# Kernel tuning notes

Hardware: AMD Instinct MI355X
Metric: run time of the kernel (lower is better)

Reference implementation:

```python
import jax, jax.numpy as jnp
import numpy as np

N_NODES = 100000
N_EDGES = 1600000
D_IN, D_HID, D_OUT = 64, 64, 32


def _glorot(key, shape):
    fan_in = shape[0]
    return jax.random.normal(key, shape, dtype=jnp.float32) / np.sqrt(fan_in)


def setup_inputs() -> dict:
    key = jax.random.key(0)
    ks = jax.random.split(key, 12)
    x = jax.random.normal(ks[0], (N_NODES, D_IN), dtype=jnp.float32)
    edge_index = jax.random.randint(ks[1], (2, N_EDGES), 0, N_NODES, dtype=jnp.int32)
    dims = [(D_IN, D_HID), (D_HID, D_HID), (D_HID, D_OUT)]
    params = {}
    for i, (din, dout) in enumerate(dims):
        params[f"Wl{i}"] = _glorot(ks[2 + 3 * i], (din, dout))
        params[f"Wr{i}"] = _glorot(ks[3 + 3 * i], (din, dout))
        params[f"b{i}"] = jnp.zeros((dout,), dtype=jnp.float32)
    return {"x": x, "edge_index": edge_index, **params}


def _sage_conv(h, src, dst, deg_inv, Wl, Wr, b):
    # mean-aggregate neighbor features: gather from src, scatter-sum to dst
    msg_sum = jax.ops.segment_sum(h[src], dst, num_segments=N_NODES)  # [N, F]
    mean = msg_sum * deg_inv[:, None]
    # lin_l(mean) + bias + lin_r(h)  (PyG SAGEConv: bias lives in lin_l)
    return mean @ Wl + b + h @ Wr


def reference(x, edge_index, Wl0, Wr0, b0, Wl1, Wr1, b1, Wl2, Wr2, b2):
    src, dst = edge_index[0], edge_index[1]
    deg = jax.ops.segment_sum(jnp.ones((N_EDGES,), x.dtype), dst, num_segments=N_NODES)
    deg_inv = 1.0 / jnp.maximum(deg, 1.0)  # mean with clamp for isolated nodes
    h = jax.nn.elu(_sage_conv(x, src, dst, deg_inv, Wl0, Wr0, b0))
    h = jax.nn.elu(_sage_conv(h, src, dst, deg_inv, Wl1, Wr1, b1))
    return _sage_conv(h, src, dst, deg_inv, Wl2, Wr2, b2)
```

## Files before the change

kernel.cpp:

```cpp
#include <hip/hip_runtime.h>
#include <cstdint>
#include <cstddef>


constexpr int SBW = 256;
constexpr int LOGSBW = 8;
constexpr int CAPS = 4608;
constexpr int CAPSP = 5632;
constexpr int CHK = 2048;

typedef __attribute__((ext_vector_type(8))) short s16x8;
typedef __attribute__((ext_vector_type(4))) float f32x4;
typedef __attribute__((ext_vector_type(2))) float f32x2;

__device__ inline unsigned short f2bf(float f) {
  unsigned u = __builtin_bit_cast(unsigned, f);
  u += 0x7FFFu + ((u >> 16) & 1u);
  return (unsigned short)(u >> 16);
}
__device__ inline float bf2f(unsigned short b) {
  unsigned u = ((unsigned)b) << 16;
  return __builtin_bit_cast(float, u);
}
__device__ inline unsigned char f2fp8(float f) {
  int p = __builtin_amdgcn_cvt_pk_fp8_f32(f, f, 0, false);
  return (unsigned char)(p & 0xFF);
}


__global__ __launch_bounds__(256) void init_ws(int* __restrict__ bcur, int NSB,
                                               const float* __restrict__ Wl0,
                                               const float* __restrict__ Wr0,
                                               const float* __restrict__ Wl1,
                                               const float* __restrict__ Wr1,
                                               const float* __restrict__ Wl2,
                                               const float* __restrict__ Wr2,
                                               unsigned short* __restrict__ Wsw) {
  const int tid = threadIdx.x;
  if (blockIdx.x == 0) {
    for (int i = tid; i < NSB; i += 256) bcur[i] = 0;
    return;
  }
  int g = (blockIdx.x - 1) * 256 + tid;
  if (g >= 10240) return;
  int s = g * 2;
  int layer, off;
  if (s < 8192)       { layer = 0; off = 0; }
  else if (s < 16384) { layer = 1; off = 8192; }
  else                { layer = 2; off = 16384; }
  int t = s - off;
  int D = (layer == 2) ? 32 : 64;
  int NTT = D / 16;
  int tt = t >> 10;
  int rem = t & 1023;
  int plane = rem >> 9;
  int rem2 = rem & 511;
  int lane = rem2 >> 3;
  int j = rem2 & 7;
  int q = lane >> 4, m = lane & 15;
  int k = plane * 32 + q * 8 + j;
  const float* W;
  int c;
  if (tt < NTT) {
    c = tt;
    W = (layer == 0) ? Wl0 : (layer == 1) ? Wl1 : Wl2;
  } else {
    c = tt - NTT;
    W = (layer == 0) ? Wr0 : (layer == 1) ? Wr1 : Wr2;
  }
  int col = c * 16 + m;
  unsigned lo = f2bf(W[k * D + col]);
  unsigned hi = f2bf(W[(k + 1) * D + col]);
  *(unsigned*)&Wsw[s] = lo | (hi << 16);
}


__global__ __launch_bounds__(256) void bin_coarse(const int* __restrict__ src,
                                                  const int* __restrict__ dst,
                                                  int* __restrict__ bcur,
                                                  unsigned int* __restrict__ coarse,
                                                  int NSB, int E) {
  __shared__ int h[512];
  __shared__ unsigned ed[CHK];
  __shared__ short sb[CHK];
  const int tid = threadIdx.x;
  for (int i = tid; i < NSB; i += 256) h[i] = 0;
  __syncthreads();
  const int e0 = blockIdx.x * CHK;
  const int e1 = min(E, e0 + CHK);
  for (int e = e0 + tid; e < e1; e += 256) {
    int d = dst[e];
    int s = src[e];
    int b = d >> LOGSBW;
    ed[e - e0] = (unsigned)s | ((unsigned)(d & (SBW - 1)) << 17);
    sb[e - e0] = (short)b;
    atomicAdd(&h[b], 1);
  }
  __syncthreads();
  for (int i = tid; i < NSB; i += 256) {
    int c = h[i];
    h[i] = c ? (i * CAPS + atomicAdd(&bcur[i], c)) : 0;
  }
  __syncthreads();
  const int n = e1 - e0;
  for (int k = tid; k < n; k += 256) {
    int b = sb[k];
    int pos = atomicAdd(&h[b], 1);
    if (pos < (b + 1) * CAPS)
      coarse[pos] = ed[k];
  }
}


__global__ __launch_bounds__(256) void csr_gemm0(const unsigned int* __restrict__ coarse,
                                                 const int* __restrict__ bcur,
                                                 int* __restrict__ rowstart,
                                                 int* __restrict__ degarr,
                                                 float* __restrict__ deg_inv,
                                                 int* __restrict__ colidx,
                                                 const float* __restrict__ x,
                                                 const unsigned short* __restrict__ Wf,
                                                 const float* __restrict__ bias,
                                                 unsigned char* __restrict__ t_out,
                                                 unsigned short* __restrict__ r_out,
                                                 int N, int NSB) {
  __shared__ int cnt[SBW];
  __shared__ int sc[SBW];
  __shared__ int cur[SBW];
  const int tid = threadIdx.x;
  if ((int)blockIdx.x < NSB) {
    const int b = blockIdx.x;
    cnt[tid] = 0;
    __syncthreads();
    const int ec = min(bcur[b], CAPS);
    const int baseC = b * CAPS;
    const int baseP = b * CAPSP;
    for (int e = tid; e < ec; e += 256)
      atomicAdd(&cnt[coarse[baseC + e] >> 17], 1);
    __syncthreads();
    int v = cnt[tid];
    int pc = (v + 3) & ~3;
    sc[tid] = pc;
    __syncthreads();
    for (int off = 1; off < SBW; off <<= 1) {
      int y = sc[tid];
      if (tid >= off) y += sc[tid - off];
      __syncthreads();
      sc[tid] = y;
      __syncthreads();
    }
    int pex = sc[tid] - pc;
    cur[tid] = pex;
    int gn = b * SBW + tid;
    if (gn < N) {
      rowstart[gn] = baseP + pex;
      degarr[gn] = pc;
      deg_inv[gn] = 1.0f / (float)(v > 1 ? v : 1);
    }
    __syncthreads();
    for (int e = tid; e < ec; e += 256) {
      unsigned p = coarse[baseC + e];
      int dl = (int)(p >> 17);
      int s = (int)(p & 0x1FFFFu);
      int l = atomicAdd(&cur[dl], 1);
      if (l < CAPSP)
        colidx[baseP + l] = s;
    }
    int pe = pex + pc;
    if (pe > CAPSP) pe = CAPSP;
    for (int l = pex + v; l < pe; ++l) colidx[baseP + l] = N;
    return;
  }
  constexpr int DOUT = 64;
  constexpr int NTT = 4;
  const int gbid = blockIdx.x - NSB;
  if (gbid == 0 && tid < 16)
    ((unsigned*)t_out)[(size_t)N * 16 + tid] = 0u;
  const int wv = tid >> 6, lane = tid & 63;
  const int q = lane >> 4, m = lane & 15;
  const int row = gbid * 64 + wv * 16 + m;
  const int rowc = row < N ? row : N - 1;
  const float* xp = &x[(size_t)rowc * 64];
  float4 f0 = *(const float4*)&xp[q * 8];
  float4 f1 = *(const float4*)&xp[q * 8 + 4];
  float4 f2 = *(const float4*)&xp[32 + q * 8];
  float4 f3 = *(const float4*)&xp[32 + q * 8 + 4];
  s16x8 a0, a1;
  a0[0] = (short)f2bf(f0.x); a0[1] = (short)f2bf(f0.y);
  a0[2] = (short)f2bf(f0.z); a0[3] = (short)f2bf(f0.w);
  a0[4] = (short)f2bf(f1.x); a0[5] = (short)f2bf(f1.y);
  a0[6] = (short)f2bf(f1.z); a0[7] = (short)f2bf(f1.w);
  a1[0] = (short)f2bf(f2.x); a1[1] = (short)f2bf(f2.y);
  a1[2] = (short)f2bf(f2.z); a1[3] = (short)f2bf(f2.w);
  a1[4] = (short)f2bf(f3.x); a1[5] = (short)f2bf(f3.y);
  a1[6] = (short)f2bf(f3.z); a1[7] = (short)f2bf(f3.w);

  f32x4 acc[2 * NTT];
#pragma unroll
  for (int c = 0; c < 2 * NTT; ++c) acc[c] = (f32x4){0.f, 0.f, 0.f, 0.f};
#pragma unroll
  for (int c = 0; c < 2 * NTT; ++c) {
    s16x8 b0 = *(const s16x8*)&Wf[(c * 2 + 0) * 512 + lane * 8];
    s16x8 b1 = *(const s16x8*)&Wf[(c * 2 + 1) * 512 + lane * 8];
    acc[c] = __builtin_amdgcn_mfma_f32_16x16x32_bf16(a0, b0, acc[c], 0, 0, 0);
    acc[c] = __builtin_amdgcn_mfma_f32_16x16x32_bf16(a1, b1, acc[c], 0, 0, 0);
  }

  const int orow = gbid * 64 + wv * 16 + q * 4;
#pragma unroll
  for (int c = 0; c < NTT; ++c) {
#pragma unroll
    for (int i = 0; i < 4; ++i) {
      int r_ = orow + i;
      if (r_ < N) t_out[(size_t)r_ * DOUT + c * 16 + m] = f2fp8(acc[c][i]);
    }
  }
#pragma unroll
  for (int c = 0; c < NTT; ++c) {
    float bv = bias[c * 16 + m];
#pragma unroll
    for (int i = 0; i < 4; ++i) {
      int r_ = orow + i;
      if (r_ < N) r_out[(size_t)r_ * DOUT + c * 16 + m] = f2bf(acc[NTT + c][i] + bv);
    }
  }
}


template <int DOUT, bool TFP8, bool RB16>
__global__ __launch_bounds__(256) void gemm_mfma(const unsigned short* __restrict__ Hm,
                                                 const unsigned short* __restrict__ Wf,
                                                 const float* __restrict__ bias,
                                                 void* __restrict__ t_out,
                                                 void* __restrict__ r_out, int N) {
  constexpr int NTT = DOUT / 16;
  constexpr int ROWB = TFP8 ? DOUT : DOUT * 2;
  const int tid = threadIdx.x;
  if (blockIdx.x == 0 && tid < ROWB / 4)
    ((unsigned*)((char*)t_out + (size_t)N * ROWB))[tid] = 0u;
  const int wv = tid >> 6, lane = tid & 63;
  const int q = lane >> 4, m = lane & 15;
  const int row = blockIdx.x * 64 + wv * 16 + m;
  const int rowc = row < N ? row : N - 1;
  const s16x8 a0 = *(const s16x8*)&Hm[(size_t)rowc * 64 + q * 8];
  const s16x8 a1 = *(const s16x8*)&Hm[(size_t)rowc * 64 + 32 + q * 8];

  f32x4 acc[2 * NTT];
#pragma unroll
  for (int c = 0; c < 2 * NTT; ++c) acc[c] = (f32x4){0.f, 0.f, 0.f, 0.f};
#pragma unroll
  for (int c = 0; c < 2 * NTT; ++c) {
    s16x8 b0 = *(const s16x8*)&Wf[(c * 2 + 0) * 512 + lane * 8];
    s16x8 b1 = *(const s16x8*)&Wf[(c * 2 + 1) * 512 + lane * 8];
    acc[c] = __builtin_amdgcn_mfma_f32_16x16x32_bf16(a0, b0, acc[c], 0, 0, 0);
    acc[c] = __builtin_amdgcn_mfma_f32_16x16x32_bf16(a1, b1, acc[c], 0, 0, 0);
  }

  const int orow = blockIdx.x * 64 + wv * 16 + q * 4;
#pragma unroll
  for (int c = 0; c < NTT; ++c) {
#pragma unroll
    for (int i = 0; i < 4; ++i) {
      int r_ = orow + i;
      if (r_ < N) {
        if (TFP8)
          ((unsigned char*)t_out)[(size_t)r_ * DOUT + c * 16 + m] = f2fp8(acc[c][i]);
        else
          ((unsigned short*)t_out)[(size_t)r_ * DOUT + c * 16 + m] = f2bf(acc[c][i]);
      }
    }
  }
#pragma unroll
  for (int c = 0; c < NTT; ++c) {
    float bv = bias[c * 16 + m];
#pragma unroll
    for (int i = 0; i < 4; ++i) {
      int r_ = orow + i;
      if (r_ < N) {
        if (RB16)
          ((unsigned short*)r_out)[(size_t)r_ * DOUT + c * 16 + m] =
              f2bf(acc[NTT + c][i] + bv);
        else
          ((float*)r_out)[(size_t)r_ * DOUT + c * 16 + m] = acc[NTT + c][i] + bv;
      }
    }
  }
}


__global__ __launch_bounds__(256) void gather_fp8(const uint2* __restrict__ t,
                                                  const unsigned short* __restrict__ r,
                                                  const float* __restrict__ deg_inv,
                                                  const int* __restrict__ rowstart,
                                                  const int* __restrict__ degarr,
                                                  const int* __restrict__ colidx,
                                                  unsigned short* __restrict__ Xout,
                                                  int N) {
  int node = blockIdx.x * 32 + (threadIdx.x >> 3);
  int lane = threadIdx.x & 7;
  if (node >= N) return;
  int b = rowstart[node];
  int e = b + degarr[node];
  float s[8];
#pragma unroll
  for (int k = 0; k < 8; ++k) s[k] = 0.f;
  int i = b;
  for (; i + 8 <= e; i += 8) {
    int4 c0 = *(const int4*)&colidx[i];
    int4 c1 = *(const int4*)&colidx[i + 4];
    uint2 v[8];
    v[0] = t[(size_t)c0.x * 8 + lane];
    v[1] = t[(size_t)c0.y * 8 + lane];
    v[2] = t[(size_t)c0.z * 8 + lane];
    v[3] = t[(size_t)c0.w * 8 + lane];
    v[4] = t[(size_t)c1.x * 8 + lane];
    v[5] = t[(size_t)c1.y * 8 + lane];
    v[6] = t[(size_t)c1.z * 8 + lane];
    v[7] = t[(size_t)c1.w * 8 + lane];
#pragma unroll
    for (int j = 0; j < 8; ++j) {
      f32x2 p0 = __builtin_amdgcn_cvt_pk_f32_fp8((int)v[j].x, false);
      f32x2 p1 = __builtin_amdgcn_cvt_pk_f32_fp8((int)v[j].x, true);
      f32x2 p2 = __builtin_amdgcn_cvt_pk_f32_fp8((int)v[j].y, false);
      f32x2 p3 = __builtin_amdgcn_cvt_pk_f32_fp8((int)v[j].y, true);
      s[0] += p0[0]; s[1] += p0[1]; s[2] += p1[0]; s[3] += p1[1];
      s[4] += p2[0]; s[5] += p2[1]; s[6] += p3[0]; s[7] += p3[1];
    }
  }
  if (i < e) {
    int4 c0 = *(const int4*)&colidx[i];
    uint2 v[4];
    v[0] = t[(size_t)c0.x * 8 + lane];
    v[1] = t[(size_t)c0.y * 8 + lane];
    v[2] = t[(size_t)c0.z * 8 + lane];
    v[3] = t[(size_t)c0.w * 8 + lane];
#pragma unroll
    for (int j = 0; j < 4; ++j) {
      f32x2 p0 = __builtin_amdgcn_cvt_pk_f32_fp8((int)v[j].x, false);
      f32x2 p1 = __builtin_amdgcn_cvt_pk_f32_fp8((int)v[j].x, true);
      f32x2 p2 = __builtin_amdgcn_cvt_pk_f32_fp8((int)v[j].y, false);
      f32x2 p3 = __builtin_amdgcn_cvt_pk_f32_fp8((int)v[j].y, true);
      s[0] += p0[0]; s[1] += p0[1]; s[2] += p1[0]; s[3] += p1[1];
      s[4] += p2[0]; s[5] += p2[1]; s[6] += p3[0]; s[7] += p3[1];
    }
  }
  float dv = deg_inv[node];
  const s16x8 rv = *(const s16x8*)&r[(size_t)node * 64 + lane * 8];
  float a[8];
#pragma unroll
  for (int k = 0; k < 8; ++k) a[k] = s[k] * dv + bf2f((unsigned short)rv[k]);
  s16x8 hv;
#pragma unroll
  for (int k = 0; k < 8; ++k) {
    float ak = a[k] > 0.f ? a[k] : (expf(a[k]) - 1.f);
    hv[k] = (short)f2bf(ak);
  }
  *(s16x8*)&Xout[(size_t)node * 64 + lane * 8] = hv;
}


__global__ __launch_bounds__(256) void gather_out(const uint2* __restrict__ t,
                                                  const float* __restrict__ r,
                                                  const float* __restrict__ deg_inv,
                                                  const int* __restrict__ rowstart,
                                                  const int* __restrict__ degarr,
                                                  const int* __restrict__ colidx,
                                                  float* __restrict__ out, int N) {
  constexpr int L = 8;
  int node = blockIdx.x * 32 + threadIdx.x / L;
  int lane = threadIdx.x & (L - 1);
  if (node >= N) return;
  int b = rowstart[node];
  int e = b + degarr[node];
  float s0 = 0.f, s1 = 0.f, s2 = 0.f, s3 = 0.f;
  int i = b;
  for (; i + 8 <= e; i += 8) {
    int4 c0 = *(const int4*)&colidx[i];
    int4 c1 = *(const int4*)&colidx[i + 4];
    uint2 v[8];
    v[0] = t[(size_t)c0.x * L + lane];
    v[1] = t[(size_t)c0.y * L + lane];
    v[2] = t[(size_t)c0.z * L + lane];
    v[3] = t[(size_t)c0.w * L + lane];
    v[4] = t[(size_t)c1.x * L + lane];
    v[5] = t[(size_t)c1.y * L + lane];
    v[6] = t[(size_t)c1.z * L + lane];
    v[7] = t[(size_t)c1.w * L + lane];
#pragma unroll
    for (int j = 0; j < 8; ++j) {
      s0 += bf2f((unsigned short)(v[j].x & 0xFFFFu));
      s1 += bf2f((unsigned short)(v[j].x >> 16));
      s2 += bf2f((unsigned short)(v[j].y & 0xFFFFu));
      s3 += bf2f((unsigned short)(v[j].y >> 16));
    }
  }
  if (i < e) {
    int4 c0 = *(const int4*)&colidx[i];
    uint2 v[4];
    v[0] = t[(size_t)c0.x * L + lane];
    v[1] = t[(size_t)c0.y * L + lane];
    v[2] = t[(size_t)c0.z * L + lane];
    v[3] = t[(size_t)c0.w * L + lane];
#pragma unroll
    for (int j = 0; j < 4; ++j) {
      s0 += bf2f((unsigned short)(v[j].x & 0xFFFFu));
      s1 += bf2f((unsigned short)(v[j].x >> 16));
      s2 += bf2f((unsigned short)(v[j].y & 0xFFFFu));
      s3 += bf2f((unsigned short)(v[j].y >> 16));
    }
  }
  float dv = deg_inv[node];
  float4 rv = *(const float4*)&r[(size_t)node * 32 + 4 * lane];
  *(float4*)&out[(size_t)node * 32 + 4 * lane] =
      make_float4(s0 * dv + rv.x, s1 * dv + rv.y, s2 * dv + rv.z, s3 * dv + rv.w);
}


extern "C" void kernel_launch(void* const* d_in, const int* in_sizes, int n_in,
                              void* d_out, int out_size, void* d_ws, size_t ws_size,
                              hipStream_t stream) {
  const float* x   = (const float*)d_in[0];
  const int*   ei  = (const int*)d_in[1];
  const float* Wl0 = (const float*)d_in[2];
  const float* Wr0 = (const float*)d_in[3];
  const float* b0  = (const float*)d_in[4];
  const float* Wl1 = (const float*)d_in[5];
  const float* Wr1 = (const float*)d_in[6];
  const float* b1  = (const float*)d_in[7];
  const float* Wl2 = (const float*)d_in[8];
  const float* Wr2 = (const float*)d_in[9];
  const float* b2  = (const float*)d_in[10];
  float* out = (float*)d_out;

  const int N = in_sizes[0] / 64;
  const int E = in_sizes[1] / 2;
  const int* srcv = ei;
  const int* dstv = ei + E;
  const int NSB = (N + SBW - 1) >> LOGSBW;

  auto al = [](size_t v) { return (v + 255) & ~(size_t)255; };
  char* w = (char*)d_ws;
  size_t oBcur = 0;
  size_t oRow  = oBcur + al(4 * (size_t)NSB);
  size_t oDeg  = oRow + al(4 * (size_t)N);
  size_t oDinv = oDeg + al(4 * (size_t)N);
  size_t oWsw  = oDinv + al(4 * (size_t)N);
  size_t oBin  = oWsw + al(2 * 20480);
  size_t oCol  = oBin + al(4 * (size_t)NSB * CAPS);
  size_t oP8   = oCol + al(4 * (size_t)NSB * CAPSP);
  size_t oP16  = oP8 + al((size_t)(N + 1) * 64);
  size_t oX    = oP16 + al((size_t)(N + 1) * 64);
  size_t oR    = oX + al(2 * (size_t)N * 64);

  int*            bcur     = (int*)(w + oBcur);
  int*            rowstart = (int*)(w + oRow);
  int*            degarr   = (int*)(w + oDeg);
  float*          deg_inv  = (float*)(w + oDinv);
  unsigned short* Wsw      = (unsigned short*)(w + oWsw);
  unsigned*       coarse   = (unsigned*)(w + oBin);
  int*            colidx   = (int*)(w + oCol);
  unsigned char*  P8       = (unsigned char*)(w + oP8);
  unsigned short* P16      = (unsigned short*)(w + oP16);
  unsigned short* X        = (unsigned short*)(w + oX);
  unsigned short* Rb       = (unsigned short*)(w + oR);
  float*          Rf       = (float*)(w + oR);

  int bbl = (E + CHK - 1) / CHK;
  int gb = (N + 63) / 64;
  int ggb = (N + 31) / 32;

  init_ws<<<41, 256, 0, stream>>>(bcur, NSB, Wl0, Wr0, Wl1, Wr1, Wl2, Wr2, Wsw);
  bin_coarse<<<bbl, 256, 0, stream>>>(srcv, dstv, bcur, coarse, NSB, E);
  csr_gemm0<<<NSB + gb, 256, 0, stream>>>(coarse, bcur, rowstart, degarr,
                                          deg_inv, colidx, x, Wsw, b0, P8, Rb,
                                          N, NSB);
  gather_fp8<<<ggb, 256, 0, stream>>>((const uint2*)P8, Rb, deg_inv, rowstart,
                                      degarr, colidx, X, N);
  gemm_mfma<64, true, true><<<gb, 256, 0, stream>>>(X, Wsw + 8192, b1, P8, Rb, N);
  gather_fp8<<<ggb, 256, 0, stream>>>((const uint2*)P8, Rb, deg_inv, rowstart,
                                      degarr, colidx, X, N);
  gemm_mfma<32, false, false><<<gb, 256, 0, stream>>>(X, Wsw + 16384, b2, P16, Rf, N);
  gather_out<<<ggb, 256, 0, stream>>>((const uint2*)P16, Rf, deg_inv, rowstart,
                                      degarr, colidx, out, N);
}
```

Baseline: 242.7 us.

## Degree-sort gather nodes via packed metadata, prefetch colidx, merge weight swizzle into binning

Within each 256-node superblock, nodes are counting-sorted by degree into a packed int4 metadata array (rowstart, padded degree, true degree, node id). The gather kernels walk this array so lanes in a wavefront get similar trip counts, and they compute deg_inv inline instead of loading it. Column indices are software-prefetched one iteration ahead with nontemporal loads. The weight-swizzle work moves into the binning launch, leaving only a tiny zeroing kernel. The extra indirection scatters output writes and costs some shared-memory atomics and scans in the CSR build.

```diff
diff --git a/kernel.cpp b/kernel.cpp
--- a/kernel.cpp
+++ b/kernel.cpp
@@ -12,6 +12,7 @@
 typedef __attribute__((ext_vector_type(8))) short s16x8;
 typedef __attribute__((ext_vector_type(4))) float f32x4;
 typedef __attribute__((ext_vector_type(2))) float f32x2;
+typedef __attribute__((ext_vector_type(4))) int i32x4;
 
 __device__ inline unsigned short f2bf(float f) {
   unsigned u = __builtin_bit_cast(unsigned, f);
@@ -28,62 +29,62 @@
 }
 
 
-__global__ __launch_bounds__(256) void init_ws(int* __restrict__ bcur, int NSB,
-                                               const float* __restrict__ Wl0,
-                                               const float* __restrict__ Wr0,
-                                               const float* __restrict__ Wl1,
-                                               const float* __restrict__ Wr1,
-                                               const float* __restrict__ Wl2,
-                                               const float* __restrict__ Wr2,
-                                               unsigned short* __restrict__ Wsw) {
-  const int tid = threadIdx.x;
-  if (blockIdx.x == 0) {
-    for (int i = tid; i < NSB; i += 256) bcur[i] = 0;
-    return;
-  }
-  int g = (blockIdx.x - 1) * 256 + tid;
-  if (g >= 10240) return;
-  int s = g * 2;
-  int layer, off;
-  if (s < 8192)       { layer = 0; off = 0; }
-  else if (s < 16384) { layer = 1; off = 8192; }
-  else                { layer = 2; off = 16384; }
-  int t = s - off;
-  int D = (layer == 2) ? 32 : 64;
-  int NTT = D / 16;
-  int tt = t >> 10;
-  int rem = t & 1023;
-  int plane = rem >> 9;
-  int rem2 = rem & 511;
-  int lane = rem2 >> 3;
-  int j = rem2 & 7;
-  int q = lane >> 4, m = lane & 15;
-  int k = plane * 32 + q * 8 + j;
-  const float* W;
-  int c;
-  if (tt < NTT) {
-    c = tt;
-    W = (layer == 0) ? Wl0 : (layer == 1) ? Wl1 : Wl2;
-  } else {
-    c = tt - NTT;
-    W = (layer == 0) ? Wr0 : (layer == 1) ? Wr1 : Wr2;
-  }
-  int col = c * 16 + m;
-  unsigned lo = f2bf(W[k * D + col]);
-  unsigned hi = f2bf(W[(k + 1) * D + col]);
-  *(unsigned*)&Wsw[s] = lo | (hi << 16);
-}
-
-
-__global__ __launch_bounds__(256) void bin_coarse(const int* __restrict__ src,
-                                                  const int* __restrict__ dst,
-                                                  int* __restrict__ bcur,
-                                                  unsigned int* __restrict__ coarse,
-                                                  int NSB, int E) {
+__global__ __launch_bounds__(256) void zero_bcur(int* __restrict__ bcur, int NSB) {
+  for (int i = threadIdx.x; i < NSB; i += 256) bcur[i] = 0;
+}
+
+
+__global__ __launch_bounds__(256) void bin_stage(const int* __restrict__ src,
+                                                 const int* __restrict__ dst,
+                                                 int* __restrict__ bcur,
+                                                 unsigned int* __restrict__ coarse,
+                                                 int NSB, int E,
+                                                 const float* __restrict__ Wl0,
+                                                 const float* __restrict__ Wr0,
+                                                 const float* __restrict__ Wl1,
+                                                 const float* __restrict__ Wr1,
+                                                 const float* __restrict__ Wl2,
+                                                 const float* __restrict__ Wr2,
+                                                 unsigned short* __restrict__ Wsw) {
   __shared__ int h[512];
   __shared__ unsigned ed[CHK];
   __shared__ short sb[CHK];
   const int tid = threadIdx.x;
+  const int bbl = (E + CHK - 1) / CHK;
+  if ((int)blockIdx.x >= bbl) {
+    int g = (blockIdx.x - bbl) * 256 + tid;
+    if (g >= 10240) return;
+    int s = g * 2;
+    int layer, off;
+    if (s < 8192)       { layer = 0; off = 0; }
+    else if (s < 16384) { layer = 1; off = 8192; }
+    else                { layer = 2; off = 16384; }
+    int t = s - off;
+    int D = (layer == 2) ? 32 : 64;
+    int NTT = D / 16;
+    int tt = t >> 10;
+    int rem = t & 1023;
+    int plane = rem >> 9;
+    int rem2 = rem & 511;
+    int lane = rem2 >> 3;
+    int j = rem2 & 7;
+    int q = lane >> 4, m = lane & 15;
+    int k = plane * 32 + q * 8 + j;
+    const float* W;
+    int c;
+    if (tt < NTT) {
+      c = tt;
+      W = (layer == 0) ? Wl0 : (layer == 1) ? Wl1 : Wl2;
+    } else {
+      c = tt - NTT;
+      W = (layer == 0) ? Wr0 : (layer == 1) ? Wr1 : Wr2;
+    }
+    int col = c * 16 + m;
+    unsigned lo = f2bf(W[k * D + col]);
+    unsigned hi = f2bf(W[(k + 1) * D + col]);
+    *(unsigned*)&Wsw[s] = lo | (hi << 16);
+    return;
+  }
   for (int i = tid; i < NSB; i += 256) h[i] = 0;
   __syncthreads();
   const int e0 = blockIdx.x * CHK;
@@ -114,9 +115,7 @@
 
 __global__ __launch_bounds__(256) void csr_gemm0(const unsigned int* __restrict__ coarse,
                                                  const int* __restrict__ bcur,
-                                                 int* __restrict__ rowstart,
-                                                 int* __restrict__ degarr,
-                                                 float* __restrict__ deg_inv,
+                                                 int4* __restrict__ metaS,
                                                  int* __restrict__ colidx,
                                                  const float* __restrict__ x,
                                                  const unsigned short* __restrict__ Wf,
@@ -127,10 +126,14 @@
   __shared__ int cnt[SBW];
   __shared__ int sc[SBW];
   __shared__ int cur[SBW];
+  __shared__ int hist[64];
+  __shared__ int sc64[64];
+  __shared__ int hcur[64];
   const int tid = threadIdx.x;
   if ((int)blockIdx.x < NSB) {
     const int b = blockIdx.x;
     cnt[tid] = 0;
+    if (tid < 64) hist[tid] = 0;
     __syncthreads();
     const int ec = min(bcur[b], CAPS);
     const int baseC = b * CAPS;
@@ -141,6 +144,10 @@
     int v = cnt[tid];
     int pc = (v + 3) & ~3;
     sc[tid] = pc;
+    const int gn = b * SBW + tid;
+    const bool valid = gn < N;
+    const int d = valid ? (v < 62 ? v : 62) : 63;
+    atomicAdd(&hist[d], 1);
     __syncthreads();
     for (int off = 1; off < SBW; off <<= 1) {
       int y = sc[tid];
@@ -151,13 +158,19 @@
     }
     int pex = sc[tid] - pc;
     cur[tid] = pex;
-    int gn = b * SBW + tid;
-    if (gn < N) {
-      rowstart[gn] = baseP + pex;
-      degarr[gn] = pc;
-      deg_inv[gn] = 1.0f / (float)(v > 1 ? v : 1);
-    }
+    if (tid < 64) sc64[tid] = hist[tid];
     __syncthreads();
+    for (int off = 1; off < 64; off <<= 1) {
+      int y = 0;
+      if (tid < 64) { y = sc64[tid]; if (tid >= off) y += sc64[tid - off]; }
+      __syncthreads();
+      if (tid < 64) sc64[tid] = y;
+      __syncthreads();
+    }
+    if (tid < 64) hcur[tid] = sc64[tid] - hist[tid];
+    __syncthreads();
+    int rank = atomicAdd(&hcur[d], 1);
+    metaS[b * SBW + rank] = make_int4(baseP + pex, pc | (v << 16), gn, 0);
     for (int e = tid; e < ec; e += 256) {
       unsigned p = coarse[baseC + e];
       int dl = (int)(p >> 17);
@@ -221,7 +234,7 @@
 #pragma unroll
     for (int i = 0; i < 4; ++i) {
       int r_ = orow + i;
-      if (r_ < N) r_out[(size_t)r_ * DOUT + c * 16 + m] = f2bf(acc[NTT + c][i] + bv);
+      if (r_ < N) r_out[(size_t)r_ * 64 + c * 16 + m] = f2bf(acc[NTT + c][i] + bv);
     }
   }
 }
@@ -290,45 +303,50 @@
 
 __global__ __launch_bounds__(256) void gather_fp8(const uint2* __restrict__ t,
                                                   const unsigned short* __restrict__ r,
-                                                  const float* __restrict__ deg_inv,
-                                                  const int* __restrict__ rowstart,
-                                                  const int* __restrict__ degarr,
+                                                  const int4* __restrict__ metaS,
                                                   const int* __restrict__ colidx,
                                                   unsigned short* __restrict__ Xout,
                                                   int N) {
-  int node = blockIdx.x * 32 + (threadIdx.x >> 3);
-  int lane = threadIdx.x & 7;
+  const int slot = blockIdx.x * 32 + ((int)threadIdx.x >> 3);
+  const int lane = threadIdx.x & 7;
+  const int4 mt = metaS[slot];
+  const int node = mt.z;
   if (node >= N) return;
-  int b = rowstart[node];
-  int e = b + degarr[node];
+  const int b = mt.x;
+  const int pc = mt.y & 0xFFFF;
+  const int vr = mt.y >> 16;
+  const int e = b + pc;
   float s[8];
 #pragma unroll
   for (int k = 0; k < 8; ++k) s[k] = 0.f;
   int i = b;
-  for (; i + 8 <= e; i += 8) {
-    int4 c0 = *(const int4*)&colidx[i];
-    int4 c1 = *(const int4*)&colidx[i + 4];
+  i32x4 c0 = __builtin_nontemporal_load((const i32x4*)&colidx[i]);
+  i32x4 c1 = __builtin_nontemporal_load((const i32x4*)&colidx[i + 4]);
+  for (; i + 8 <= e;) {
+    i32x4 p0 = c0, p1 = c1;
+    i += 8;
+    c0 = __builtin_nontemporal_load((const i32x4*)&colidx[i]);
+    c1 = __builtin_nontemporal_load((const i32x4*)&colidx[i + 4]);
     uint2 v[8];
-    v[0] = t[(size_t)c0.x * 8 + lane];
-    v[1] = t[(size_t)c0.y * 8 + lane];
-    v[2] = t[(size_t)c0.z * 8 + lane];
-    v[3] = t[(size_t)c0.w * 8 + lane];
-    v[4] = t[(size_t)c1.x * 8 + lane];
-    v[5] = t[(size_t)c1.y * 8 + lane];
-    v[6] = t[(size_t)c1.z * 8 + lane];
-    v[7] = t[(size_t)c1.w * 8 + lane];
+    v[0] = t[(size_t)p0.x * 8 + lane];
+    v[1] = t[(size_t)p0.y * 8 + lane];
+    v[2] = t[(size_t)p0.z * 8 + lane];
+    v[3] = t[(size_t)p0.w * 8 + lane];
+    v[4] = t[(size_t)p1.x * 8 + lane];
+    v[5] = t[(size_t)p1.y * 8 + lane];
+    v[6] = t[(size_t)p1.z * 8 + lane];
+    v[7] = t[(size_t)p1.w * 8 + lane];
 #pragma unroll
     for (int j = 0; j < 8; ++j) {
-      f32x2 p0 = __builtin_amdgcn_cvt_pk_f32_fp8((int)v[j].x, false);
-      f32x2 p1 = __builtin_amdgcn_cvt_pk_f32_fp8((int)v[j].x, true);
-      f32x2 p2 = __builtin_amdgcn_cvt_pk_f32_fp8((int)v[j].y, false);
-      f32x2 p3 = __builtin_amdgcn_cvt_pk_f32_fp8((int)v[j].y, true);
-      s[0] += p0[0]; s[1] += p0[1]; s[2] += p1[0]; s[3] += p1[1];
-      s[4] += p2[0]; s[5] += p2[1]; s[6] += p3[0]; s[7] += p3[1];
+      f32x2 p0f = __builtin_amdgcn_cvt_pk_f32_fp8((int)v[j].x, false);
+      f32x2 p1f = __builtin_amdgcn_cvt_pk_f32_fp8((int)v[j].x, true);
+      f32x2 p2f = __builtin_amdgcn_cvt_pk_f32_fp8((int)v[j].y, false);
+      f32x2 p3f = __builtin_amdgcn_cvt_pk_f32_fp8((int)v[j].y, true);
+      s[0] += p0f[0]; s[1] += p0f[1]; s[2] += p1f[0]; s[3] += p1f[1];
+      s[4] += p2f[0]; s[5] += p2f[1]; s[6] += p3f[0]; s[7] += p3f[1];
     }
   }
   if (i < e) {
-    int4 c0 = *(const int4*)&colidx[i];
     uint2 v[4];
     v[0] = t[(size_t)c0.x * 8 + lane];
     v[1] = t[(size_t)c0.y * 8 + lane];
@@ -336,23 +354,21 @@
     v[3] = t[(size_t)c0.w * 8 + lane];
 #pragma unroll
     for (int j = 0; j < 4; ++j) {
-      f32x2 p0 = __builtin_amdgcn_cvt_pk_f32_fp8((int)v[j].x, false);
-      f32x2 p1 = __builtin_amdgcn_cvt_pk_f32_fp8((int)v[j].x, true);
-      f32x2 p2 = __builtin_amdgcn_cvt_pk_f32_fp8((int)v[j].y, false);
-      f32x2 p3 = __builtin_amdgcn_cvt_pk_f32_fp8((int)v[j].y, true);
-      s[0] += p0[0]; s[1] += p0[1]; s[2] += p1[0]; s[3] += p1[1];
-      s[4] += p2[0]; s[5] += p2[1]; s[6] += p3[0]; s[7] += p3[1];
-    }
-  }
-  float dv = deg_inv[node];
+      f32x2 p0f = __builtin_amdgcn_cvt_pk_f32_fp8((int)v[j].x, false);
+      f32x2 p1f = __builtin_amdgcn_cvt_pk_f32_fp8((int)v[j].x, true);
+      f32x2 p2f = __builtin_amdgcn_cvt_pk_f32_fp8((int)v[j].y, false);
+      f32x2 p3f = __builtin_amdgcn_cvt_pk_f32_fp8((int)v[j].y, true);
+      s[0] += p0f[0]; s[1] += p0f[1]; s[2] += p1f[0]; s[3] += p1f[1];
+      s[4] += p2f[0]; s[5] += p2f[1]; s[6] += p3f[0]; s[7] += p3f[1];
+    }
+  }
+  const float dv = 1.0f / (float)(vr > 1 ? vr : 1);
   const s16x8 rv = *(const s16x8*)&r[(size_t)node * 64 + lane * 8];
-  float a[8];
-#pragma unroll
-  for (int k = 0; k < 8; ++k) a[k] = s[k] * dv + bf2f((unsigned short)rv[k]);
   s16x8 hv;
 #pragma unroll
   for (int k = 0; k < 8; ++k) {
-    float ak = a[k] > 0.f ? a[k] : (expf(a[k]) - 1.f);
+    float ak = s[k] * dv + bf2f((unsigned short)rv[k]);
+    ak = ak > 0.f ? ak : (expf(ak) - 1.f);
     hv[k] = (short)f2bf(ak);
   }
   *(s16x8*)&Xout[(size_t)node * 64 + lane * 8] = hv;
@@ -361,31 +377,36 @@
 
 __global__ __launch_bounds__(256) void gather_out(const uint2* __restrict__ t,
                                                   const float* __restrict__ r,
-                                                  const float* __restrict__ deg_inv,
-                                                  const int* __restrict__ rowstart,
-                                                  const int* __restrict__ degarr,
+                                                  const int4* __restrict__ metaS,
                                                   const int* __restrict__ colidx,
                                                   float* __restrict__ out, int N) {
-  constexpr int L = 8;
-  int node = blockIdx.x * 32 + threadIdx.x / L;
-  int lane = threadIdx.x & (L - 1);
+  const int slot = blockIdx.x * 32 + ((int)threadIdx.x >> 3);
+  const int lane = threadIdx.x & 7;
+  const int4 mt = metaS[slot];
+  const int node = mt.z;
   if (node >= N) return;
-  int b = rowstart[node];
-  int e = b + degarr[node];
+  const int b = mt.x;
+  const int pc = mt.y & 0xFFFF;
+  const int vr = mt.y >> 16;
+  const int e = b + pc;
   float s0 = 0.f, s1 = 0.f, s2 = 0.f, s3 = 0.f;
   int i = b;
-  for (; i + 8 <= e; i += 8) {
-    int4 c0 = *(const int4*)&colidx[i];
-    int4 c1 = *(const int4*)&colidx[i + 4];
+  i32x4 c0 = __builtin_nontemporal_load((const i32x4*)&colidx[i]);
+  i32x4 c1 = __builtin_nontemporal_load((const i32x4*)&colidx[i + 4]);
+  for (; i + 8 <= e;) {
+    i32x4 p0 = c0, p1 = c1;
+    i += 8;
+    c0 = __builtin_nontemporal_load((const i32x4*)&colidx[i]);
+    c1 = __builtin_nontemporal_load((const i32x4*)&colidx[i + 4]);
     uint2 v[8];
-    v[0] = t[(size_t)c0.x * L + lane];
-    v[1] = t[(size_t)c0.y * L + lane];
-    v[2] = t[(size_t)c0.z * L + lane];
-    v[3] = t[(size_t)c0.w * L + lane];
-    v[4] = t[(size_t)c1.x * L + lane];
-    v[5] = t[(size_t)c1.y * L + lane];
-    v[6] = t[(size_t)c1.z * L + lane];
-    v[7] = t[(size_t)c1.w * L + lane];
+    v[0] = t[(size_t)p0.x * 8 + lane];
+    v[1] = t[(size_t)p0.y * 8 + lane];
+    v[2] = t[(size_t)p0.z * 8 + lane];
+    v[3] = t[(size_t)p0.w * 8 + lane];
+    v[4] = t[(size_t)p1.x * 8 + lane];
+    v[5] = t[(size_t)p1.y * 8 + lane];
+    v[6] = t[(size_t)p1.z * 8 + lane];
+    v[7] = t[(size_t)p1.w * 8 + lane];
 #pragma unroll
     for (int j = 0; j < 8; ++j) {
       s0 += bf2f((unsigned short)(v[j].x & 0xFFFFu));
@@ -395,12 +416,11 @@
     }
   }
   if (i < e) {
-    int4 c0 = *(const int4*)&colidx[i];
     uint2 v[4];
-    v[0] = t[(size_t)c0.x * L + lane];
-    v[1] = t[(size_t)c0.y * L + lane];
-    v[2] = t[(size_t)c0.z * L + lane];
-    v[3] = t[(size_t)c0.w * L + lane];
+    v[0] = t[(size_t)c0.x * 8 + lane];
+    v[1] = t[(size_t)c0.y * 8 + lane];
+    v[2] = t[(size_t)c0.z * 8 + lane];
+    v[3] = t[(size_t)c0.w * 8 + lane];
 #pragma unroll
     for (int j = 0; j < 4; ++j) {
       s0 += bf2f((unsigned short)(v[j].x & 0xFFFFu));
@@ -409,7 +429,7 @@
       s3 += bf2f((unsigned short)(v[j].y >> 16));
     }
   }
-  float dv = deg_inv[node];
+  const float dv = 1.0f / (float)(vr > 1 ? vr : 1);
   float4 rv = *(const float4*)&r[(size_t)node * 32 + 4 * lane];
   *(float4*)&out[(size_t)node * 32 + 4 * lane] =
       make_float4(s0 * dv + rv.x, s1 * dv + rv.y, s2 * dv + rv.z, s3 * dv + rv.w);
@@ -437,14 +457,13 @@
   const int* srcv = ei;
   const int* dstv = ei + E;
   const int NSB = (N + SBW - 1) >> LOGSBW;
+  const int SLOTS = NSB * SBW;
 
   auto al = [](size_t v) { return (v + 255) & ~(size_t)255; };
   char* w = (char*)d_ws;
   size_t oBcur = 0;
-  size_t oRow  = oBcur + al(4 * (size_t)NSB);
-  size_t oDeg  = oRow + al(4 * (size_t)N);
-  size_t oDinv = oDeg + al(4 * (size_t)N);
-  size_t oWsw  = oDinv + al(4 * (size_t)N);
+  size_t oMeta = oBcur + al(4 * (size_t)NSB);
+  size_t oWsw  = oMeta + al(16 * (size_t)SLOTS);
   size_t oBin  = oWsw + al(2 * 20480);
   size_t oCol  = oBin + al(4 * (size_t)NSB * CAPS);
   size_t oP8   = oCol + al(4 * (size_t)NSB * CAPSP);
@@ -453,9 +472,7 @@
   size_t oR    = oX + al(2 * (size_t)N * 64);
 
   int*            bcur     = (int*)(w + oBcur);
-  int*            rowstart = (int*)(w + oRow);
-  int*            degarr   = (int*)(w + oDeg);
-  float*          deg_inv  = (float*)(w + oDinv);
+  int4*           metaS    = (int4*)(w + oMeta);
   unsigned short* Wsw      = (unsigned short*)(w + oWsw);
   unsigned*       coarse   = (unsigned*)(w + oBin);
   int*            colidx   = (int*)(w + oCol);
@@ -467,19 +484,16 @@
 
   int bbl = (E + CHK - 1) / CHK;
   int gb = (N + 63) / 64;
-  int ggb = (N + 31) / 32;
-
-  init_ws<<<41, 256, 0, stream>>>(bcur, NSB, Wl0, Wr0, Wl1, Wr1, Wl2, Wr2, Wsw);
-  bin_coarse<<<bbl, 256, 0, stream>>>(srcv, dstv, bcur, coarse, NSB, E);
-  csr_gemm0<<<NSB + gb, 256, 0, stream>>>(coarse, bcur, rowstart, degarr,
-                                          deg_inv, colidx, x, Wsw, b0, P8, Rb,
-                                          N, NSB);
-  gather_fp8<<<ggb, 256, 0, stream>>>((const uint2*)P8, Rb, deg_inv, rowstart,
-                                      degarr, colidx, X, N);
+  int ggb = SLOTS / 32;
+
+  zero_bcur<<<1, 256, 0, stream>>>(bcur, NSB);
+  bin_stage<<<bbl + 40, 256, 0, stream>>>(srcv, dstv, bcur, coarse, NSB, E,
+                                          Wl0, Wr0, Wl1, Wr1, Wl2, Wr2, Wsw);
+  csr_gemm0<<<NSB + gb, 256, 0, stream>>>(coarse, bcur, metaS, colidx, x, Wsw,
+                                          b0, P8, Rb, N, NSB);
+  gather_fp8<<<ggb, 256, 0, stream>>>((const uint2*)P8, Rb, metaS, colidx, X, N);
   gemm_mfma<64, true, true><<<gb, 256, 0, stream>>>(X, Wsw + 8192, b1, P8, Rb, N);
-  gather_fp8<<<ggb, 256, 0, stream>>>((const uint2*)P8, Rb, deg_inv, rowstart,
-                                      degarr, colidx, X, N);
+  gather_fp8<<<ggb, 256, 0, stream>>>((const uint2*)P8, Rb, metaS, colidx, X, N);
   gemm_mfma<32, false, false><<<gb, 256, 0, stream>>>(X, Wsw + 16384, b2, P16, Rf, N);
-  gather_out<<<ggb, 256, 0, stream>>>((const uint2*)P16, Rf, deg_inv, rowstart,
-                                      degarr, colidx, out, N);
-}
+  gather_out<<<ggb, 256, 0, stream>>>((const uint2*)P16, Rf, metaS, colidx, out, N);
+}
```

Result: slower. 278.3 us (+14.7%).
